# Kernel tuning notes

Measured on AMD Instinct MI355X. Metric: run time of the kernel, lower is better.

## Reference

```python
import jax, jax.numpy as jnp
import numpy as np

MARGIN = 1.0


def setup_inputs() -> dict:
    key = jax.random.key(0)
    k1, k2 = jax.random.split(key)
    B, D = 8192, 128
    embedding = jax.random.normal(k1, (B, D), dtype=jnp.float32)
    target = jax.random.randint(k2, (B,), 0, 64, dtype=jnp.int64)
    return {"embedding": embedding, "target": target}


def reference(embedding, target):
    B = embedding.shape[0]
    # Pairwise Euclidean distances (cdist), used only for mining -> no grad.
    sq = jnp.sum(embedding * embedding, axis=1)                       # [B]
    d2 = sq[:, None] + sq[None, :] - 2.0 * (embedding @ embedding.T)  # [B, B]
    dist = jnp.sqrt(jnp.maximum(d2, 0.0))
    dist = jax.lax.stop_gradient(dist)

    same = target[:, None] == target[None, :]                         # [B, B]
    not_self = ~jnp.eye(B, dtype=bool)
    pos_mask = same & not_self
    neg_mask = ~same

    # Batch-hard mining: hardest (farthest) positive, hardest (closest) negative.
    pos_idx = jnp.argmax(jnp.where(pos_mask, dist, -jnp.inf), axis=1)  # [B]
    neg_idx = jnp.argmin(jnp.where(neg_mask, dist, jnp.inf), axis=1)   # [B]

    a = embedding
    p = embedding[pos_idx]
    n = embedding[neg_idx]

    dp = jnp.linalg.norm(a - p, axis=1)  # [B]
    dn = jnp.linalg.norm(a - n, axis=1)  # [B]
    loss = jax.nn.relu(dp - dn + MARGIN)
    return jnp.mean(loss)
```

## Files before the change

kernel.cpp:

```cpp
#include <hip/hip_runtime.h>
#include <hip/hip_bf16.h>
#include <math.h>

#define BN 8192
#define DK 128
#define NSPLIT 16
#define JR (BN / NSPLIT)
#define NG (JR / 128)
#define MARGIN_F 1.0f

#define OFF_EBS  524288
#define OFF_SQ   1048576
#define OFF_POSV (OFF_SQ + BN)
#define OFF_NEGV (OFF_POSV + NSPLIT * BN)
#define OFF_RED  (OFF_NEGV + NSPLIT * BN)

typedef __attribute__((ext_vector_type(8))) short bf16x8;
typedef __attribute__((ext_vector_type(4))) float f32x4;

__device__ __forceinline__ unsigned short f2bf(float f) {
    __hip_bfloat16 h = __float2bfloat16(f);
    return *reinterpret_cast<unsigned short*>(&h);
}

__device__ __forceinline__ void gload_lds16(const void* g, void* s) {
    __builtin_amdgcn_global_load_lds(
        (const __attribute__((address_space(1))) void*)g,
        (__attribute__((address_space(3))) void*)s, 16, 0, 0);
}

__global__ __launch_bounds__(256) void k_prep(const float* __restrict__ emb,
                                              unsigned short* __restrict__ Eb,
                                              unsigned short* __restrict__ EbS,
                                              float* __restrict__ sq64) {
    int row  = blockIdx.x * 4 + (threadIdx.x >> 6);
    int lane = threadIdx.x & 63;
    float2 v = ((const float2*)(emb + (size_t)row * DK))[lane];
    ushort2 o;  o.x  = f2bf(v.x);           o.y  = f2bf(v.y);
    ushort2 os; os.x = f2bf(v.x * -128.0f); os.y = f2bf(v.y * -128.0f);
    ((ushort2*)(Eb  + (size_t)row * DK))[lane] = o;
    ((ushort2*)(EbS + (size_t)row * DK))[lane] = os;
    float s = v.x * v.x + v.y * v.y;
    #pragma unroll
    for (int m = 32; m; m >>= 1) s += __shfl_xor(s, m);
    if (lane == 0) sq64[row] = 64.0f * s;
}

__global__ __launch_bounds__(256)
void k_mine8(const unsigned short* __restrict__ Eb,
             const unsigned short* __restrict__ EbS,
             const float* __restrict__ sq64,
             const int* __restrict__ tgt,
             float* __restrict__ posV, float* __restrict__ negV) {
    __shared__ __align__(16) char Blds[2][2][16384];

    const int tid = threadIdx.x;
    const int w   = tid >> 6;
    const int l   = tid & 63;
    const int lh  = l >> 4;
    const int tx  = l & 15;
    const int igroup = blockIdx.x >> 4;
    const int split  = blockIdx.x & 15;
    const int i0w = igroup * 256 + w * 64;
    const int jb  = split * JR;
    const char* EbB = (const char*)Eb;

    bf16x8 A[4][4];
    #pragma unroll
    for (int mi = 0; mi < 4; ++mi) {
        const char* rp = (const char*)EbS + (size_t)(i0w + mi * 16 + tx) * 256 + lh * 16;
        #pragma unroll
        for (int ks = 0; ks < 4; ++ks)
            A[mi][ks] = *(const bf16x8*)(rp + ks * 64);
    }

    int t8[16];
    #pragma unroll
    for (int mi = 0; mi < 4; ++mi) {
        int4 q = *(const int4*)(tgt + i0w + mi * 16 + lh * 4);
        t8[mi * 4 + 0] = q.x; t8[mi * 4 + 1] = q.y;
        t8[mi * 4 + 2] = q.z; t8[mi * 4 + 3] = q.w;
    }

    float pp[16], nn[16];
    #pragma unroll
    for (int r = 0; r < 16; ++r) { pp[r] = -INFINITY; nn[r] = INFINITY; }

    auto stage64 = [&](char* dst, int jcol0) {
        const char* S = EbB + (size_t)jcol0 * 256;
        #pragma unroll
        for (int q = 0; q < 4; ++q) {
            int f  = tid + 256 * q;
            int gr = f >> 4;
            int sc = (f & 15) ^ (gr & 7);
            gload_lds16(S + gr * 256 + sc * 16, dst + w * 1024 + q * 4096);
        }
    };

    stage64(Blds[0][0], jb);
    stage64(Blds[0][1], jb + 64);
    __syncthreads();

    for (int g = 0; g < NG; ++g) {
        const int buf = g & 1;
        if (g + 1 < NG) {
            stage64(Blds[buf ^ 1][0], jb + (g + 1) * 128);
            stage64(Blds[buf ^ 1][1], jb + (g + 1) * 128 + 64);
        }
        const int j0 = jb + g * 128;

        float sqv[4][2]; int tjv[4][2];
        #pragma unroll
        for (int s = 0; s < 4; ++s)
            #pragma unroll
            for (int u = 0; u < 2; ++u) {
                int j = j0 + s * 32 + u * 16 + tx;
                sqv[s][u] = sq64[j]; tjv[s][u] = tgt[j];
            }

        #pragma unroll
        for (int s = 0; s < 4; ++s) {
            f32x4 acc[4][2];
            #pragma unroll
            for (int mi = 0; mi < 4; ++mi)
                #pragma unroll
                for (int u = 0; u < 2; ++u) {
                    float sv = sqv[s][u];
                    f32x4 a0 = {sv, sv, sv, sv};
                    acc[mi][u] = a0;
                }

            const char* base = Blds[buf][s >> 1];
            #pragma unroll
            for (int ks = 0; ks < 4; ++ks) {
                bf16x8 Bf[2];
                #pragma unroll
                for (int u = 0; u < 2; ++u) {
                    int row = (s & 1) * 32 + u * 16 + tx;
                    int c   = (ks * 4 + lh) ^ (row & 7);
                    Bf[u] = *(const bf16x8*)(base + row * 256 + c * 16);
                }
                __builtin_amdgcn_s_setprio(1);
                #pragma unroll
                for (int mi = 0; mi < 4; ++mi)
                    #pragma unroll
                    for (int u = 0; u < 2; ++u)
                        acc[mi][u] = __builtin_amdgcn_mfma_f32_16x16x32_bf16(
                            A[mi][ks], Bf[u], acc[mi][u], 0, 0, 0);
                __builtin_amdgcn_s_setprio(0);
            }

            const int tj0 = tjv[s][0], tj1 = tjv[s][1];
            #pragma unroll
            for (int mi = 0; mi < 4; ++mi) {
                #pragma unroll
                for (int v = 0; v < 4; ++v) {
                    const int r = mi * 4 + v;
                    const int trg = t8[r];
                    float k0 = acc[mi][0][v];
                    float k1 = acc[mi][1][v];
                    bool s0 = (tj0 == trg);
                    bool s1 = (tj1 == trg);
                    float a0 = s0 ? k0 : -INFINITY;
                    float b0 = s0 ? INFINITY : k0;
                    float a1 = s1 ? k1 : -INFINITY;
                    float b1 = s1 ? INFINITY : k1;
                    pp[r] = fmaxf(fmaxf(pp[r], a0), a1);
                    nn[r] = fminf(fminf(nn[r], b0), b1);
                }
            }
        }

        __syncthreads();
    }

    #pragma unroll
    for (int r = 0; r < 16; ++r) {
        float p = pp[r], n = nn[r];
        #pragma unroll
        for (int m = 1; m < 16; m <<= 1) {
            p = fmaxf(p, __shfl_xor(p, m));
            n = fminf(n, __shfl_xor(n, m));
        }
        if (tx == 0) {
            int row = i0w + (r >> 2) * 16 + lh * 4 + (r & 3);
            posV[split * BN + row] = p;
            negV[split * BN + row] = n;
        }
    }
}

__global__ __launch_bounds__(256) void k_finm(const float* __restrict__ sq64,
                                              const float* __restrict__ posV,
                                              const float* __restrict__ negV,
                                              unsigned long long* __restrict__ red,
                                              float* __restrict__ out) {
    int row  = blockIdx.x * 256 + threadIdx.x;
    int lane = threadIdx.x & 63;

    float p = -INFINITY, n = INFINITY;
    #pragma unroll
    for (int s = 0; s < NSPLIT; ++s) {
        p = fmaxf(p, posV[s * BN + row]);
        n = fminf(n, negV[s * BN + row]);
    }
    float s64 = sq64[row];
    float d2p = fmaxf(p + s64, 0.f) * 0.015625f;
    float d2n = fmaxf(n + s64, 0.f) * 0.015625f;
    float lo  = sqrtf(d2p) - sqrtf(d2n) + MARGIN_F;
    lo = lo > 0.f ? lo : 0.f;

    #pragma unroll
    for (int m = 32; m; m >>= 1) lo += __shfl_xor(lo, m);
    __shared__ float part[4];
    if (lane == 0) part[threadIdx.x >> 6] = lo;
    __syncthreads();
    if (threadIdx.x == 0) {
        float bs = part[0] + part[1] + part[2] + part[3];
        atomicAdd(red, (unsigned long long)(bs * 16777216.0f));
        __threadfence();
        unsigned int t = atomicAdd((unsigned int*)(red + 1), 1u);
        if (t == gridDim.x - 1) {
            unsigned long long tot = atomicAdd(red, 0ULL);
            out[0] = (float)((double)tot / 16777216.0 / (double)BN);
        }
    }
}

extern "C" void kernel_launch(void* const* d_in, const int* in_sizes, int n_in,
                              void* d_out, int out_size, void* d_ws, size_t ws_size,
                              hipStream_t stream) {
    const float* emb = (const float*)d_in[0];
    const int*   tgt = (const int*)d_in[1];
    float* out = (float*)d_out;

    float* wsf = (float*)d_ws;
    unsigned short* Eb  = (unsigned short*)wsf;
    unsigned short* EbS = (unsigned short*)(wsf + OFF_EBS);
    float* sq64 = wsf + OFF_SQ;
    float* posV = wsf + OFF_POSV;
    float* negV = wsf + OFF_NEGV;
    unsigned long long* red = (unsigned long long*)(wsf + OFF_RED);

    hipMemsetAsync(red, 0, 16, stream);
    k_prep<<<BN / 4, 256, 0, stream>>>(emb, Eb, EbS, sq64);
    k_mine8<<<(BN / 256) * NSPLIT, 256, 0, stream>>>(Eb, EbS, sq64, tgt, posV, negV);
    k_finm<<<BN / 256, 256, 0, stream>>>(sq64, posV, negV, red, out);
}
```

Measured before the change: 44.84 us.

## Exploit distance matrix symmetry by computing only upper-triangular 256x256 tiles

The mining kernel now launches one block per upper-triangular 256x256 tile (528 tiles instead of 512 full-row blocks covering 8192x512). Each off-diagonal tile reduces both row-wise and column-wise hardest positive/negative, writing column results through shared memory to the transposed slot. This roughly halves the MFMA and B-operand load work. It adds per-element column reductions, shuffles and an LDS pass, and the finalize kernel now reads 32 partial slots instead of 16. The row squared norm is also folded into the mined value so finalize no longer reads it.

```diff
diff --git a/kernel.cpp b/kernel.cpp
--- a/kernel.cpp
+++ b/kernel.cpp
@@ -4,16 +4,15 @@
 
 #define BN 8192
 #define DK 128
-#define NSPLIT 16
-#define JR (BN / NSPLIT)
-#define NG (JR / 128)
+#define NSLOT 32
+#define NTILES (NSLOT * (NSLOT + 1) / 2)
 #define MARGIN_F 1.0f
 
 #define OFF_EBS  524288
 #define OFF_SQ   1048576
 #define OFF_POSV (OFF_SQ + BN)
-#define OFF_NEGV (OFF_POSV + NSPLIT * BN)
-#define OFF_RED  (OFF_NEGV + NSPLIT * BN)
+#define OFF_NEGV (OFF_POSV + NSLOT * BN)
+#define OFF_RED  (OFF_NEGV + NSLOT * BN)
 
 typedef __attribute__((ext_vector_type(8))) short bf16x8;
 typedef __attribute__((ext_vector_type(4))) float f32x4;
@@ -47,22 +46,26 @@
 }
 
 __global__ __launch_bounds__(256)
-void k_mine8(const unsigned short* __restrict__ Eb,
+void k_mine9(const unsigned short* __restrict__ Eb,
              const unsigned short* __restrict__ EbS,
              const float* __restrict__ sq64,
              const int* __restrict__ tgt,
              float* __restrict__ posV, float* __restrict__ negV) {
     __shared__ __align__(16) char Blds[2][2][16384];
+    __shared__ float colP[4][256], colN[4][256];
 
     const int tid = threadIdx.x;
     const int w   = tid >> 6;
     const int l   = tid & 63;
     const int lh  = l >> 4;
     const int tx  = l & 15;
-    const int igroup = blockIdx.x >> 4;
-    const int split  = blockIdx.x & 15;
-    const int i0w = igroup * 256 + w * 64;
-    const int jb  = split * JR;
+
+    int I = 0, rem = blockIdx.x;
+    while (rem >= NSLOT - I) { rem -= NSLOT - I; ++I; }
+    const int J = I + rem;
+    const bool diag = (I == J);
+    const int i0w = I * 256 + w * 64;
+    const int jb  = J * 256;
     const char* EbB = (const char*)Eb;
 
     bf16x8 A[4][4];
@@ -74,9 +77,12 @@
             A[mi][ks] = *(const bf16x8*)(rp + ks * 64);
     }
 
-    int t8[16];
+    float si[16]; int t8[16];
     #pragma unroll
     for (int mi = 0; mi < 4; ++mi) {
+        float4 s4 = *(const float4*)(sq64 + i0w + mi * 16 + lh * 4);
+        si[mi * 4 + 0] = s4.x; si[mi * 4 + 1] = s4.y;
+        si[mi * 4 + 2] = s4.z; si[mi * 4 + 3] = s4.w;
         int4 q = *(const int4*)(tgt + i0w + mi * 16 + lh * 4);
         t8[mi * 4 + 0] = q.x; t8[mi * 4 + 1] = q.y;
         t8[mi * 4 + 2] = q.z; t8[mi * 4 + 3] = q.w;
@@ -101,11 +107,10 @@
     stage64(Blds[0][1], jb + 64);
     __syncthreads();
 
-    for (int g = 0; g < NG; ++g) {
-        const int buf = g & 1;
-        if (g + 1 < NG) {
-            stage64(Blds[buf ^ 1][0], jb + (g + 1) * 128);
-            stage64(Blds[buf ^ 1][1], jb + (g + 1) * 128 + 64);
+    for (int g = 0; g < 2; ++g) {
+        if (g == 0) {
+            stage64(Blds[1][0], jb + 128);
+            stage64(Blds[1][1], jb + 192);
         }
         const int j0 = jb + g * 128;
 
@@ -130,7 +135,7 @@
                     acc[mi][u] = a0;
                 }
 
-            const char* base = Blds[buf][s >> 1];
+            const char* base = Blds[g][s >> 1];
             #pragma unroll
             for (int ks = 0; ks < 4; ++ks) {
                 bf16x8 Bf[2];
@@ -151,22 +156,43 @@
             }
 
             const int tj0 = tjv[s][0], tj1 = tjv[s][1];
+            float pc0 = -INFINITY, pc1 = -INFINITY;
+            float nc0 =  INFINITY, nc1 =  INFINITY;
             #pragma unroll
             for (int mi = 0; mi < 4; ++mi) {
                 #pragma unroll
                 for (int v = 0; v < 4; ++v) {
                     const int r = mi * 4 + v;
                     const int trg = t8[r];
-                    float k0 = acc[mi][0][v];
-                    float k1 = acc[mi][1][v];
+                    float v0 = acc[mi][0][v] + si[r];
+                    float v1 = acc[mi][1][v] + si[r];
                     bool s0 = (tj0 == trg);
                     bool s1 = (tj1 == trg);
-                    float a0 = s0 ? k0 : -INFINITY;
-                    float b0 = s0 ? INFINITY : k0;
-                    float a1 = s1 ? k1 : -INFINITY;
-                    float b1 = s1 ? INFINITY : k1;
+                    float a0 = s0 ? v0 : -INFINITY;
+                    float b0 = s0 ?  INFINITY : v0;
+                    float a1 = s1 ? v1 : -INFINITY;
+                    float b1 = s1 ?  INFINITY : v1;
                     pp[r] = fmaxf(fmaxf(pp[r], a0), a1);
                     nn[r] = fminf(fminf(nn[r], b0), b1);
+                    if (!diag) {
+                        pc0 = fmaxf(pc0, a0); pc1 = fmaxf(pc1, a1);
+                        nc0 = fminf(nc0, b0); nc1 = fminf(nc1, b1);
+                    }
+                }
+            }
+            if (!diag) {
+                pc0 = fmaxf(pc0, __shfl_xor(pc0, 16));
+                pc0 = fmaxf(pc0, __shfl_xor(pc0, 32));
+                pc1 = fmaxf(pc1, __shfl_xor(pc1, 16));
+                pc1 = fmaxf(pc1, __shfl_xor(pc1, 32));
+                nc0 = fminf(nc0, __shfl_xor(nc0, 16));
+                nc0 = fminf(nc0, __shfl_xor(nc0, 32));
+                nc1 = fminf(nc1, __shfl_xor(nc1, 16));
+                nc1 = fminf(nc1, __shfl_xor(nc1, 32));
+                if (lh == 0) {
+                    int c0 = g * 128 + s * 32 + tx;
+                    colP[w][c0]      = pc0; colN[w][c0]      = nc0;
+                    colP[w][c0 + 16] = pc1; colN[w][c0 + 16] = nc1;
                 }
             }
         }
@@ -184,14 +210,23 @@
         }
         if (tx == 0) {
             int row = i0w + (r >> 2) * 16 + lh * 4 + (r & 3);
-            posV[split * BN + row] = p;
-            negV[split * BN + row] = n;
-        }
-    }
-}
-
-__global__ __launch_bounds__(256) void k_finm(const float* __restrict__ sq64,
-                                              const float* __restrict__ posV,
+            posV[J * BN + row] = p;
+            negV[J * BN + row] = n;
+        }
+    }
+
+    if (!diag) {
+        int c = tid;
+        float p = fmaxf(fmaxf(colP[0][c], colP[1][c]),
+                        fmaxf(colP[2][c], colP[3][c]));
+        float n = fminf(fminf(colN[0][c], colN[1][c]),
+                        fminf(colN[2][c], colN[3][c]));
+        posV[I * BN + jb + c] = p;
+        negV[I * BN + jb + c] = n;
+    }
+}
+
+__global__ __launch_bounds__(256) void k_finm(const float* __restrict__ posV,
                                               const float* __restrict__ negV,
                                               unsigned long long* __restrict__ red,
                                               float* __restrict__ out) {
@@ -200,13 +235,12 @@
 
     float p = -INFINITY, n = INFINITY;
     #pragma unroll
-    for (int s = 0; s < NSPLIT; ++s) {
+    for (int s = 0; s < NSLOT; ++s) {
         p = fmaxf(p, posV[s * BN + row]);
         n = fminf(n, negV[s * BN + row]);
     }
-    float s64 = sq64[row];
-    float d2p = fmaxf(p + s64, 0.f) * 0.015625f;
-    float d2n = fmaxf(n + s64, 0.f) * 0.015625f;
+    float d2p = fmaxf(p, 0.f) * 0.015625f;
+    float d2n = fmaxf(n, 0.f) * 0.015625f;
     float lo  = sqrtf(d2p) - sqrtf(d2n) + MARGIN_F;
     lo = lo > 0.f ? lo : 0.f;
 
@@ -244,6 +278,6 @@
 
     hipMemsetAsync(red, 0, 16, stream);
     k_prep<<<BN / 4, 256, 0, stream>>>(emb, Eb, EbS, sq64);
-    k_mine8<<<(BN / 256) * NSPLIT, 256, 0, stream>>>(Eb, EbS, sq64, tgt, posV, negV);
-    k_finm<<<BN / 256, 256, 0, stream>>>(sq64, posV, negV, red, out);
-}
+    k_mine9<<<NTILES, 256, 0, stream>>>(Eb, EbS, sq64, tgt, posV, negV);
+    k_finm<<<BN / 256, 256, 0, stream>>>(posV, negV, red, out);
+}
```

Measured after the change: 84.40 us. 88.2% more time.
